# Performance work log

Measured on AMD Instinct MI355X. Metric: run time of the kernel, lower is better.

## Reference

```python
import jax, jax.numpy as jnp
import numpy as np

WS = 8          # window_size
NH = 8          # num_heads
DIM = 512
INNER = 512
CDIM = 128
CINNER = 128
SHIFTED = True
EPS = 1e-6
N = WS * WS     # tokens per window
SCALE = 1.0 / np.sqrt(INNER // NH + CINNER // NH)  # SDPA scale over fused (feat+coord) head dim


def _rmsnorm(x, g):
    return x * jax.lax.rsqrt(jnp.mean(x * x, axis=-1, keepdims=True) + EPS) * g


def _rel_indices():
    idx = np.array([[x, y] for x in range(WS) for y in range(WS)])
    ri = idx[None, :, :] - idx[:, None, :] + WS - 1
    return ri[..., 0], ri[..., 1]


def _shift_mask(Wh, Ww):
    s = WS
    k = s * (s // 2)
    row = np.zeros((N, N), np.float32)
    row[-k:, :-k] = -np.inf
    row[:-k, -k:] = -np.inf
    col = row.reshape(s, s, s, s).transpose(1, 0, 3, 2).reshape(N, N)
    m = np.zeros((Wh, Ww, N, N), np.float32)
    m[:, -1] += row
    m[-1, :] += col
    return jnp.asarray(m)


def setup_inputs() -> dict:
    key = jax.random.key(0)
    ks = jax.random.split(key, 16)
    B, h, w = 4, 128, 128

    def lin(k, fan_in, fan_out):
        return jax.random.normal(k, (fan_in, fan_out), jnp.float32) * (fan_in ** -0.5)

    return {
        "features": jax.random.normal(ks[0], (B, h, w, DIM), jnp.float32),
        "coords": jax.random.normal(ks[1], (B, h, w, CDIM), jnp.float32),
        "w_fqk": lin(ks[2], DIM, 2 * INNER),
        "b_fqk": jnp.zeros((2 * INNER,), jnp.float32),
        "g_fqk": jnp.ones((2 * INNER,), jnp.float32),
        "w_cqk": lin(ks[3], CDIM, 2 * CINNER),
        "b_cqk": jnp.zeros((2 * CINNER,), jnp.float32),
        "g_cqk": jnp.ones((2 * CINNER,), jnp.float32),
        "w_v": lin(ks[4], DIM, INNER),
        "b_v": jnp.zeros((INNER,), jnp.float32),
        "w_out": lin(ks[5], INNER, DIM),
        "b_out": jnp.zeros((DIM,), jnp.float32),
        "pos_emb": jax.random.normal(ks[6], (2 * WS - 1, 2 * WS - 1), jnp.float32),
    }


def reference(features, coords, w_fqk, b_fqk, g_fqk, w_cqk, b_cqk, g_cqk,
              w_v, b_v, w_out, b_out, pos_emb):
    B, h, w, _ = features.shape
    pad_h = (WS - h % WS) % WS
    pad_w = (WS - w % WS) % WS
    H_pad, W_pad = h + pad_h, w + pad_w
    Wh, Ww = H_pad // WS, W_pad // WS

    fqk = _rmsnorm(features @ w_fqk + b_fqk, g_fqk)
    f_q, f_k = jnp.split(fqk, 2, axis=-1)
    cqk = _rmsnorm(coords @ w_cqk + b_cqk, g_cqk)
    c_q, c_k = jnp.split(cqk, 2, axis=-1)
    f_v = features @ w_v + b_v

    def win(t):
        t = jnp.pad(t, ((0, 0), (0, pad_h), (0, pad_w), (0, 0)))
        if SHIFTED:
            t = jnp.roll(t, (-(WS // 2), -(WS // 2)), axis=(1, 2))
        D = t.shape[-1]
        t = t.reshape(B, Wh, WS, Ww, WS, D).transpose(0, 1, 3, 2, 4, 5)
        return t.reshape(B, Wh, Ww, N, D)

    def heads(t):
        D = t.shape[-1]
        return t.reshape(B, Wh, Ww, N, NH, D // NH)

    fq, fk, fv = heads(win(f_q)), heads(win(f_k)), heads(win(f_v))
    cq, ck = heads(win(c_q)), heads(win(c_k))

    # fused feature + coordinate QK scores, per head per window
    scores = (jnp.einsum('bxyqhd,bxykhd->bxyhqk', fq, fk)
              + jnp.einsum('bxyqhd,bxykhd->bxyhqk', cq, ck)) * SCALE

    ri0, ri1 = _rel_indices()
    pos_bias = pos_emb[ri0, ri1]  # (N, N)
    bias = pos_bias[None, None, None, None]
    if SHIFTED:
        bias = bias + _shift_mask(Wh, Ww)[None, :, :, None]
    scores = scores + bias

    attn = jax.nn.softmax(scores, axis=-1)
    out = jnp.einsum('bxyhqk,bxykhd->bxyqhd', attn, fv)
    out = out.reshape(B, Wh, Ww, N, INNER)

    # un-window
    out = out.reshape(B, Wh, Ww, WS, WS, INNER).transpose(0, 1, 3, 2, 4, 5)
    out = out.reshape(B, H_pad, W_pad, INNER)
    if SHIFTED:
        out = jnp.roll(out, (WS // 2, WS // 2), axis=(1, 2))
    out = out[:, :h, :w, :]
    return out @ w_out + b_out
```

## Files before the change

### kernel.cpp

```cpp
#include <hip/hip_runtime.h>
#include <hip/hip_bf16.h>
#include <type_traits>

using bf16 = __hip_bfloat16;
typedef __bf16 bf16x8 __attribute__((ext_vector_type(8)));
typedef float f32x4 __attribute__((ext_vector_type(4)));

static constexpr int TOKENS = 4 * 128 * 128;
#define SCALE_F 0.11180339887498949f
#define EPS_F 1e-6f

__device__ __forceinline__ float u2f(unsigned short u) {
  union { unsigned int i; float f; } c; c.i = (unsigned int)u << 16; return c.f;
}
__device__ __forceinline__ unsigned short f2u(float f) {
  bf16 h = __float2bfloat16(f); return *reinterpret_cast<unsigned short*>(&h);
}
__device__ __forceinline__ float b2f(bf16 v) { return __bfloat162float(v); }
__device__ __forceinline__ int4 cvt8(const float* p) {
  float4 a = ((const float4*)p)[0], b = ((const float4*)p)[1];
  union { int4 i4; unsigned short s[8]; } u;
  u.s[0] = f2u(a.x); u.s[1] = f2u(a.y); u.s[2] = f2u(a.z); u.s[3] = f2u(a.w);
  u.s[4] = f2u(b.x); u.s[5] = f2u(b.y); u.s[6] = f2u(b.z); u.s[7] = f2u(b.w);
  return u.i4;
}
__device__ __forceinline__ void gload16(const bf16* g, bf16* l) {
  __builtin_amdgcn_global_load_lds(
      (const __attribute__((address_space(1))) unsigned int*)g,
      (__attribute__((address_space(3))) unsigned int*)l, 16, 0, 0);
}

__global__ void convert_k(const float* __restrict__ in, bf16* __restrict__ out,
                          long n) {
  long i = ((long)blockIdx.x * 256 + threadIdx.x) * 8;
  long stride = (long)gridDim.x * 256 * 8;
  for (; i < n; i += stride) *(int4*)(out + i) = cvt8(in + i);
}

__global__ void transpose_k(const float* __restrict__ in, bf16* __restrict__ out,
                            int K, int N) {
  int i = blockIdx.x * 256 + threadIdx.x;
  if (i >= K * N) return;
  int k = i / N, n = i - k * N;
  out[(size_t)n * K + k] = __float2bfloat16(in[i]);
}

__global__ void biascat_k(const float* __restrict__ a, const float* __restrict__ b,
                          float* __restrict__ o) {
  int i = blockIdx.x * 256 + threadIdx.x;
  if (i < 1536) o[i] = i < 1024 ? a[i] : b[i - 1024];
}

template <int QF>
__device__ __forceinline__ void mfma16(f32x4 (&acc)[8][4], const bf16x8 (&wfr)[4],
                                       const bf16x8 (&xfr)[4]) {
#pragma unroll
  for (int fi = 0; fi < 4; ++fi)
#pragma unroll
    for (int j = 0; j < 4; ++j)
      acc[QF * 4 + fi][j] =
          __builtin_amdgcn_mfma_f32_16x16x32_bf16(wfr[fi], xfr[j], acc[QF * 4 + fi][j], 0, 0, 0);
}

template <typename TC, int SSNX>
__global__ __launch_bounds__(512, 2) void gemm256_k(
    const bf16* __restrict__ A, const bf16* __restrict__ Wt,
    const float* __restrict__ bias, TC* __restrict__ C,
    float* __restrict__ ssq, int M, int N, int K) {
  extern __shared__ __align__(16) bf16 smem[];
  bf16* sX = smem;
  bf16* sW = smem + 24576;
  const int t = threadIdx.x, lane = t & 63, wave = t >> 6;
  const int wm = wave >> 2, wn = wave & 3;
  const int l15 = lane & 15, kg = lane >> 4;
  const int nwg = gridDim.x * gridDim.y;
  int id = blockIdx.y * gridDim.x + blockIdx.x;
  id = (id & 7) * (nwg >> 3) + (id >> 3);
  const int bx = id % gridDim.x, by = id / gridDim.x;
  const int bm = by * 256, bn = bx * 256;
  f32x4 acc[8][4] = {};

  const int srow = t >> 2;
  const int sw8 = ((t & 3) ^ ((srow >> 1) & 3)) * 8;
  const int sdst = srow * 32 + (t & 3) * 8;
  const int fsw = (kg ^ ((l15 >> 1) & 3)) * 8;

  auto stageX = [&](int buf, int k0) {
    bf16* d = sX + buf * 8192 + sdst;
    gload16(A + (size_t)(bm + srow) * K + k0 + sw8, d);
    gload16(A + (size_t)(bm + 128 + srow) * K + k0 + sw8, d + 4096);
  };
  auto stageW = [&](int buf, int k0) {
    bf16* d = sW + buf * 8192 + sdst;
    gload16(Wt + (size_t)(bn + srow) * K + k0 + sw8, d);
    gload16(Wt + (size_t)(bn + 128 + srow) * K + k0 + sw8, d + 4096);
  };

  const int NT = K >> 5;
  stageX(0, 0); stageW(0, 0); stageX(1, 32); stageW(1, 32);

  int buf = 0;
  for (int u = 0; u < NT; ++u) {
    if (u < NT - 1) asm volatile("s_waitcnt vmcnt(4)" ::: "memory");
    else            asm volatile("s_waitcnt vmcnt(0)" ::: "memory");
    __builtin_amdgcn_s_barrier();
    __builtin_amdgcn_sched_barrier(0);
    int nb = buf + 2; if (nb >= 3) nb -= 3;
    if (u + 2 < NT) stageX(nb, (u + 2) * 32);
    bf16x8 xfr[4], wfr[4];
    const bf16* bX = sX + buf * 8192;
    const bf16* bW = sW + buf * 8192;
#pragma unroll
    for (int j = 0; j < 4; ++j)
      xfr[j] = *(const bf16x8*)(bX + (wn * 64 + j * 16 + l15) * 32 + fsw);
#pragma unroll
    for (int fi = 0; fi < 4; ++fi)
      wfr[fi] = *(const bf16x8*)(bW + (wm * 128 + fi * 16 + l15) * 32 + fsw);
    __builtin_amdgcn_s_setprio(1);
    mfma16<0>(acc, wfr, xfr);
    __builtin_amdgcn_s_setprio(0);
    if (u + 2 < NT) stageW(nb, (u + 2) * 32);
#pragma unroll
    for (int fi = 0; fi < 4; ++fi)
      wfr[fi] = *(const bf16x8*)(bW + (wm * 128 + 64 + fi * 16 + l15) * 32 + fsw);
    __builtin_amdgcn_s_setprio(1);
    mfma16<1>(acc, wfr, xfr);
    __builtin_amdgcn_s_setprio(0);
    buf = (buf == 2) ? 0 : buf + 1;
  }

  float bvi[8][4];
#pragma unroll
  for (int i = 0; i < 8; ++i) {
    float4 b4 = *(const float4*)(bias + bn + wm * 128 + (i >> 2) * 64 + (i & 3) * 16 + kg * 4);
    bvi[i][0] = b4.x; bvi[i][1] = b4.y; bvi[i][2] = b4.z; bvi[i][3] = b4.w;
  }
#pragma unroll
  for (int j = 0; j < 4; ++j) {
    const int token = bm + wn * 64 + j * 16 + l15;
    float ssum = 0.f;
#pragma unroll
    for (int i = 0; i < 8; ++i) {
      float v0 = acc[i][j][0] + bvi[i][0];
      float v1 = acc[i][j][1] + bvi[i][1];
      float v2 = acc[i][j][2] + bvi[i][2];
      float v3 = acc[i][j][3] + bvi[i][3];
      const size_t off = (size_t)token * N + bn + wm * 128 + (i >> 2) * 64 + (i & 3) * 16 + kg * 4;
      if constexpr (std::is_same<TC, float>::value) {
        *(float4*)(C + off) = float4{v0, v1, v2, v3};
      } else {
        ushort4 pk{f2u(v0), f2u(v1), f2u(v2), f2u(v3)};
        *(ushort4*)(C + off) = pk;
      }
      if constexpr (SSNX > 0)
        ssum += v0 * v0 + v1 * v1 + v2 * v2 + v3 * v3;
    }
    if constexpr (SSNX > 0) {
      ssum += __shfl_xor(ssum, 16);
      ssum += __shfl_xor(ssum, 32);
      if (bx < SSNX && kg == 0)
        ssq[(size_t)token * (SSNX * 2) + bx * 2 + wm] = ssum;
    }
  }
}

template <typename TC, int SSNX>
__global__ __launch_bounds__(256) void gemm128_k(
    const bf16* __restrict__ A, const bf16* __restrict__ Wt,
    const float* __restrict__ bias, TC* __restrict__ C,
    float* __restrict__ ssq, int M, int N, int K) {
  __shared__ __align__(16) bf16 sA[2][4096];
  __shared__ __align__(16) bf16 sB[2][4096];
  const int t = threadIdx.x, lane = t & 63, wave = t >> 6;
  const int wr = wave >> 1, wc = wave & 1;
  const int nwg = gridDim.x * gridDim.y;
  int id = blockIdx.y * gridDim.x + blockIdx.x;
  if ((nwg & 7) == 0) id = (id & 7) * (nwg >> 3) + (id >> 3);
  const int bx = id % gridDim.x, by = id / gridDim.x;
  const int bm = by * 128, bn = bx * 128;
  const int l15 = lane & 15, kg = lane >> 4;
  f32x4 acc[4][4] = {};

  const int srow = t >> 2;
  const int ske = ((t & 3) ^ ((srow >> 1) & 3)) * 8;
  const bf16* pA0 = A + (size_t)(bm + srow) * K + ske;
  const bf16* pA1 = A + (size_t)(bm + 64 + srow) * K + ske;
  const bf16* pB0 = Wt + (size_t)(bn + srow) * K + ske;
  const bf16* pB1 = Wt + (size_t)(bn + 64 + srow) * K + ske;
  const int wo = wave * 512;

  gload16(pA0, &sA[0][wo]);
  gload16(pA1, &sA[0][2048 + wo]);
  gload16(pB0, &sB[0][wo]);
  gload16(pB1, &sB[0][2048 + wo]);
  __syncthreads();

  const int nt = K >> 5;
  int cur = 0;
  for (int tt = 0; tt < nt; ++tt) {
    if (tt + 1 < nt) {
      pA0 += 32; pA1 += 32; pB0 += 32; pB1 += 32;
      gload16(pA0, &sA[cur ^ 1][wo]);
      gload16(pA1, &sA[cur ^ 1][2048 + wo]);
      gload16(pB0, &sB[cur ^ 1][wo]);
      gload16(pB1, &sB[cur ^ 1][2048 + wo]);
    }
    bf16x8 wf[4], xf[4];
#pragma unroll
    for (int i = 0; i < 4; ++i) {
      int frow = wc * 64 + i * 16 + l15;
      int xrow = wr * 64 + i * 16 + l15;
      wf[i] = *(const bf16x8*)(&sB[cur][frow * 32 + ((kg ^ ((frow >> 1) & 3)) * 8)]);
      xf[i] = *(const bf16x8*)(&sA[cur][xrow * 32 + ((kg ^ ((xrow >> 1) & 3)) * 8)]);
    }
#pragma unroll
    for (int i = 0; i < 4; ++i)
#pragma unroll
      for (int j = 0; j < 4; ++j)
        acc[i][j] = __builtin_amdgcn_mfma_f32_16x16x32_bf16(wf[i], xf[j], acc[i][j], 0, 0, 0);
    __syncthreads();
    cur ^= 1;
  }

  float bvi[4][4];
#pragma unroll
  for (int i = 0; i < 4; ++i) {
    float4 b4 = *(const float4*)(bias + bn + wc * 64 + i * 16 + kg * 4);
    bvi[i][0] = b4.x; bvi[i][1] = b4.y; bvi[i][2] = b4.z; bvi[i][3] = b4.w;
  }
#pragma unroll
  for (int j = 0; j < 4; ++j) {
    const int token = bm + wr * 64 + j * 16 + l15;
    float ssum = 0.f;
#pragma unroll
    for (int i = 0; i < 4; ++i) {
      float v0 = acc[i][j][0] + bvi[i][0];
      float v1 = acc[i][j][1] + bvi[i][1];
      float v2 = acc[i][j][2] + bvi[i][2];
      float v3 = acc[i][j][3] + bvi[i][3];
      const size_t off = (size_t)token * N + bn + wc * 64 + i * 16 + kg * 4;
      if constexpr (std::is_same<TC, float>::value) {
        *(float4*)(C + off) = float4{v0, v1, v2, v3};
      } else {
        ushort4 pk{f2u(v0), f2u(v1), f2u(v2), f2u(v3)};
        *(ushort4*)(C + off) = pk;
      }
      if constexpr (SSNX > 0)
        ssum += v0 * v0 + v1 * v1 + v2 * v2 + v3 * v3;
    }
    if constexpr (SSNX > 0) {
      ssum += __shfl_xor(ssum, 16);
      ssum += __shfl_xor(ssum, 32);
      if (bx < SSNX && kg == 0)
        ssq[(size_t)token * (SSNX * 2) + bx * 2 + wc] = ssum;
    }
  }
}

__global__ void finalize_rs_k(const float* __restrict__ pf,
                              const float* __restrict__ pc,
                              float* __restrict__ rsf, float* __restrict__ rsc) {
  int i = blockIdx.x * 256 + threadIdx.x;
  if (i >= TOKENS) return;
  float s = 0.f;
#pragma unroll
  for (int j = 0; j < 8; ++j) s += pf[(size_t)i * 8 + j];
  rsf[i] = rsqrtf(s * (1.f / 1024.f) + EPS_F);
  float c = 0.f;
#pragma unroll
  for (int j = 0; j < 4; ++j) c += pc[(size_t)i * 4 + j];
  rsc[i] = rsqrtf(c * (1.f / 256.f) + EPS_F);
}

__global__ __launch_bounds__(256) void attn_mfma_k(
    const bf16* __restrict__ qkv, const bf16* __restrict__ cqk,
    const float* __restrict__ pos, const float* __restrict__ g_fqk,
    const float* __restrict__ g_cqk, const float* __restrict__ rs_f,
    const float* __restrict__ rs_c, bf16* __restrict__ aout) {
  __shared__ __align__(16) bf16 sQ[64][104], sK[64][104];
  __shared__ __align__(16) bf16 sVt[64][72];
  __shared__ __align__(16) bf16 sP[64][72];
  __shared__ float sPos[15][15];
  __shared__ float sRsF[64], sRsC[64];
  const int t = threadIdx.x, lane = t & 63, wave = t >> 6;
  const int head = blockIdx.x & 7;
  const int wid = blockIdx.x >> 3;
  const int wx = wid & 15, wy = (wid >> 4) & 15, b = wid >> 8;

  for (int i = t; i < 225; i += 256) sPos[i / 15][i % 15] = pos[i];
  if (t < 64) {
    const int y = ((wy << 3) + (t >> 3) + 4) & 127;
    const int x = ((wx << 3) + (t & 7) + 4) & 127;
    const size_t tok = ((size_t)b << 14) | (y << 7) | x;
    sRsF[t] = rs_f[tok];
    sRsC[t] = rs_c[tok];
  }
  {
    const int n = t >> 2, p = t & 3;
    const int y = ((wy << 3) + (n >> 3) + 4) & 127;
    const int x = ((wx << 3) + (n & 7) + 4) & 127;
    const size_t tok = ((size_t)b << 14) | (y << 7) | x;
    const bf16* row = qkv + tok * 1536;
    const int4* qp = (const int4*)(row + head * 64 + p * 16);
    ((int4*)&sQ[n][p * 16])[0] = qp[0];
    ((int4*)&sQ[n][p * 16])[1] = qp[1];
    {
      const bf16* kpp = row + 512 + head * 64 + p * 16;
      const float* gq = g_fqk + head * 64 + p * 16;
      const float* gk = g_fqk + 512 + head * 64 + p * 16;
      union { int4 v[2]; unsigned short s[16]; } kt;
#pragma unroll
      for (int i = 0; i < 16; ++i)
        kt.s[i] = f2u(b2f(kpp[i]) * gq[i] * gk[i]);
      ((int4*)&sK[n][p * 16])[0] = kt.v[0];
      ((int4*)&sK[n][p * 16])[1] = kt.v[1];
    }
    const bf16* vp = row + 1024 + head * 64 + p * 16;
#pragma unroll
    for (int i = 0; i < 16; ++i) sVt[p * 16 + i][n] = vp[i];
    const bf16* crow = cqk + tok * 256;
    if (p == 0) {
      const int4* cp = (const int4*)(crow + head * 16);
      ((int4*)&sQ[n][64])[0] = cp[0];
      ((int4*)&sQ[n][64])[1] = cp[1];
    } else if (p == 1) {
      const bf16* ckp = crow + 128 + head * 16;
      const float* gcq = g_cqk + head * 16;
      const float* gck = g_cqk + 128 + head * 16;
      union { int4 v[2]; unsigned short s[16]; } ct;
#pragma unroll
      for (int i = 0; i < 16; ++i)
        ct.s[i] = f2u(b2f(ckp[i]) * gcq[i] * gck[i]);
      ((int4*)&sK[n][64])[0] = ct.v[0];
      ((int4*)&sK[n][64])[1] = ct.v[1];
    } else if (p == 2) {
      ((int4*)&sQ[n][80])[0] = int4{0, 0, 0, 0};
      ((int4*)&sQ[n][80])[1] = int4{0, 0, 0, 0};
    } else {
      ((int4*)&sK[n][80])[0] = int4{0, 0, 0, 0};
      ((int4*)&sK[n][80])[1] = int4{0, 0, 0, 0};
    }
  }
  __syncthreads();

  const int l15 = lane & 15, kg = lane >> 4;
  bf16x8 qa[3];
#pragma unroll
  for (int ko = 0; ko < 3; ++ko)
    qa[ko] = *(const bf16x8*)&sQ[wave * 16 + l15][ko * 32 + kg * 8];
  f32x4 saccf[4] = {}, saccc[4] = {};
#pragma unroll
  for (int j = 0; j < 4; ++j) {
#pragma unroll
    for (int ko = 0; ko < 2; ++ko) {
      bf16x8 kb = *(const bf16x8*)&sK[j * 16 + l15][ko * 32 + kg * 8];
      saccf[j] = __builtin_amdgcn_mfma_f32_16x16x32_bf16(qa[ko], kb, saccf[j], 0, 0, 0);
    }
    bf16x8 kb2 = *(const bf16x8*)&sK[j * 16 + l15][64 + kg * 8];
    saccc[j] = __builtin_amdgcn_mfma_f32_16x16x32_bf16(qa[2], kb2, saccc[j], 0, 0, 0);
  }

  const bool lastx = (wx == 15), lasty = (wy == 15);
  float rqf[4], rqc[4];
#pragma unroll
  for (int r = 0; r < 4; ++r) {
    rqf[r] = sRsF[wave * 16 + kg * 4 + r];
    rqc[r] = sRsC[wave * 16 + kg * 4 + r];
  }
  float sv[4][4], mx[4], sum[4], inv[4];
#pragma unroll
  for (int r = 0; r < 4; ++r) mx[r] = -1e30f;
#pragma unroll
  for (int j = 0; j < 4; ++j) {
    int kcol = j * 16 + l15, kh = kcol >> 3, kw = kcol & 7;
    float rkf = sRsF[kcol], rkc = sRsC[kcol];
#pragma unroll
    for (int r = 0; r < 4; ++r) {
      int q = wave * 16 + kg * 4 + r, qh = q >> 3, qw = q & 7;
      bool msk = (lastx && ((qh >= 4) != (kh >= 4))) ||
                 (lasty && ((qw >= 4) != (kw >= 4)));
      float raw = saccf[j][r] * rqf[r] * rkf + saccc[j][r] * rqc[r] * rkc;
      float val = msk ? -1e30f : raw * SCALE_F + sPos[kh - qh + 7][kw - qw + 7];
      sv[j][r] = val;
      mx[r] = fmaxf(mx[r], val);
    }
  }
#pragma unroll
  for (int m = 1; m < 16; m <<= 1)
#pragma unroll
    for (int r = 0; r < 4; ++r) mx[r] = fmaxf(mx[r], __shfl_xor(mx[r], m));
#pragma unroll
  for (int r = 0; r < 4; ++r) sum[r] = 0.f;
#pragma unroll
  for (int j = 0; j < 4; ++j) {
    int kcol = j * 16 + l15;
#pragma unroll
    for (int r = 0; r < 4; ++r) {
      float e = __expf(sv[j][r] - mx[r]);
      sum[r] += e;
      sP[wave * 16 + kg * 4 + r][kcol] = __float2bfloat16(e);
    }
  }
#pragma unroll
  for (int m = 1; m < 16; m <<= 1)
#pragma unroll
    for (int r = 0; r < 4; ++r) sum[r] += __shfl_xor(sum[r], m);
#pragma unroll
  for (int r = 0; r < 4; ++r) inv[r] = 1.f / sum[r];
  __syncthreads();

  bf16x8 pa[2];
#pragma unroll
  for (int ko = 0; ko < 2; ++ko)
    pa[ko] = *(const bf16x8*)&sP[wave * 16 + l15][ko * 32 + kg * 8];
  f32x4 oacc[4] = {};
#pragma unroll
  for (int jf = 0; jf < 4; ++jf)
#pragma unroll
    for (int ko = 0; ko < 2; ++ko) {
      bf16x8 vb = *(const bf16x8*)&sVt[jf * 16 + l15][ko * 32 + kg * 8];
      oacc[jf] = __builtin_amdgcn_mfma_f32_16x16x32_bf16(pa[ko], vb, oacc[jf], 0, 0, 0);
    }
#pragma unroll
  for (int r = 0; r < 4; ++r) {
    int q = wave * 16 + kg * 4 + r;
    const int y = ((wy << 3) + (q >> 3) + 4) & 127;
    const int x = ((wx << 3) + (q & 7) + 4) & 127;
    const size_t tok = ((size_t)b << 14) | (y << 7) | x;
    bf16* dst = aout + tok * 512 + head * 64;
#pragma unroll
    for (int jf = 0; jf < 4; ++jf)
      dst[jf * 16 + l15] = __float2bfloat16(oacc[jf][r] * inv[r]);
  }
}

extern "C" void kernel_launch(void* const* d_in, const int* in_sizes, int n_in,
                              void* d_out, int out_size, void* d_ws, size_t ws_size,
                              hipStream_t stream) {
  const float* features = (const float*)d_in[0];
  const float* coords   = (const float*)d_in[1];
  const float* w_fqk = (const float*)d_in[2];
  const float* b_fqk = (const float*)d_in[3];
  const float* g_fqk = (const float*)d_in[4];
  const float* w_cqk = (const float*)d_in[5];
  const float* b_cqk = (const float*)d_in[6];
  const float* g_cqk = (const float*)d_in[7];
  const float* w_v   = (const float*)d_in[8];
  const float* b_v   = (const float*)d_in[9];
  const float* w_out = (const float*)d_in[10];
  const float* b_out = (const float*)d_in[11];
  const float* pos_emb = (const float*)d_in[12];
  float* out = (float*)d_out;

  const int M = TOKENS;
  bf16* qkv   = (bf16*)d_ws;
  bf16* cqk   = qkv + (size_t)M * 1536;
  bf16* aout  = cqk + (size_t)M * 256;
  bf16* wcombT = aout + (size_t)M * 512;
  bf16* wcqkT  = wcombT + (size_t)1536 * 512;
  bf16* woutT  = wcqkT + 256 * 128;
  float* bias_comb = (float*)(woutT + 512 * 512);
  float* ssq_f = bias_comb + 1536;
  float* ssq_c = ssq_f + (size_t)M * 8;
  float* rs_f  = ssq_c + (size_t)M * 4;
  float* rs_c  = rs_f + M;
  bf16* fb16 = (bf16*)d_out;
  bf16* cb16 = fb16 + (size_t)M * 512;

  convert_k<<<2048, 256, 0, stream>>>(features, fb16, (long)M * 512);
  convert_k<<<1024, 256, 0, stream>>>(coords, cb16, (long)M * 128);
  transpose_k<<<(512 * 1024 + 255) / 256, 256, 0, stream>>>(w_fqk, wcombT, 512, 1024);
  transpose_k<<<(512 * 512 + 255) / 256, 256, 0, stream>>>(w_v, wcombT + (size_t)1024 * 512, 512, 512);
  transpose_k<<<(128 * 256 + 255) / 256, 256, 0, stream>>>(w_cqk, wcqkT, 128, 256);
  transpose_k<<<(512 * 512 + 255) / 256, 256, 0, stream>>>(w_out, woutT, 512, 512);
  biascat_k<<<6, 256, 0, stream>>>(b_fqk, b_v, bias_comb);

  gemm256_k<bf16, 4><<<dim3(6, 256), 512, 98304, stream>>>(fb16, wcombT, bias_comb, qkv, ssq_f, M, 1536, 512);
  gemm128_k<bf16, 2><<<dim3(2, 512), 256, 0, stream>>>(cb16, wcqkT, b_cqk, cqk, ssq_c, M, 256, 128);
  finalize_rs_k<<<TOKENS / 256, 256, 0, stream>>>(ssq_f, ssq_c, rs_f, rs_c);
  attn_mfma_k<<<4 * 16 * 16 * 8, 256, 0, stream>>>(qkv, cqk, pos_emb, g_fqk, g_cqk, rs_f, rs_c, aout);
  gemm256_k<float, 0><<<dim3(2, 256), 512, 98304, stream>>>(aout, woutT, b_out, out, nullptr, M, 512, 512);
}
```

Baseline: 385.0 us.

## Restructure 256x256 GEMM into double-buffered BK=64 four-phase ping-pong pipeline

Replaces the triple-buffered BK=32 GEMM main loop with a double-buffered BK=64 loop split into four sub-tile phases. Each phase loads one half of the W or X tile from LDS, issues the prefetch for that half of the next tile, and runs its MFMAs, with barriers between phases. The LDS layout changes to 64-element rows with an XOR swizzle, and LDS use grows from 96KB to 128KB per block. The goal is better overlap of global loads with MFMA work and fewer barriers per K element. The cost is more LDS per block, which may limit occupancy below the 2 blocks per CU requested by the launch bounds.

```diff
diff --git a/kernel.cpp b/kernel.cpp
--- a/kernel.cpp
+++ b/kernel.cpp
@@ -51,25 +51,14 @@
   if (i < 1536) o[i] = i < 1024 ? a[i] : b[i - 1024];
 }
 
-template <int QF>
-__device__ __forceinline__ void mfma16(f32x4 (&acc)[8][4], const bf16x8 (&wfr)[4],
-                                       const bf16x8 (&xfr)[4]) {
-#pragma unroll
-  for (int fi = 0; fi < 4; ++fi)
-#pragma unroll
-    for (int j = 0; j < 4; ++j)
-      acc[QF * 4 + fi][j] =
-          __builtin_amdgcn_mfma_f32_16x16x32_bf16(wfr[fi], xfr[j], acc[QF * 4 + fi][j], 0, 0, 0);
-}
-
 template <typename TC, int SSNX>
-__global__ __launch_bounds__(512, 2) void gemm256_k(
+__global__ __launch_bounds__(512, 2) void gemm256p_k(
     const bf16* __restrict__ A, const bf16* __restrict__ Wt,
     const float* __restrict__ bias, TC* __restrict__ C,
     float* __restrict__ ssq, int M, int N, int K) {
   extern __shared__ __align__(16) bf16 smem[];
-  bf16* sX = smem;
-  bf16* sW = smem + 24576;
+  bf16* sW = smem;
+  bf16* sX = smem + 32768;
   const int t = threadIdx.x, lane = t & 63, wave = t >> 6;
   const int wm = wave >> 2, wn = wave & 3;
   const int l15 = lane & 15, kg = lane >> 4;
@@ -80,72 +69,131 @@
   const int bm = by * 256, bn = bx * 256;
   f32x4 acc[8][4] = {};
 
-  const int srow = t >> 2;
-  const int sw8 = ((t & 3) ^ ((srow >> 1) & 3)) * 8;
-  const int sdst = srow * 32 + (t & 3) * 8;
-  const int fsw = (kg ^ ((l15 >> 1) & 3)) * 8;
-
-  auto stageX = [&](int buf, int k0) {
-    bf16* d = sX + buf * 8192 + sdst;
-    gload16(A + (size_t)(bm + srow) * K + k0 + sw8, d);
-    gload16(A + (size_t)(bm + 128 + srow) * K + k0 + sw8, d + 4096);
+  const int lr = t >> 3, ch = t & 7;
+  const int ssw = ((ch ^ (lr & 7)) * 8);
+  const int rsw = (l15 & 7) * 8;
+
+  auto stW = [&](int buf, int fh, int k0) {
+#pragma unroll
+    for (int g = 0; g < 2; ++g)
+      gload16(Wt + (size_t)(bn + g * 128 + fh * 64 + lr) * K + k0 + ssw,
+              sW + buf * 16384 + (fh * 128 + g * 64) * 64 + t * 8);
   };
-  auto stageW = [&](int buf, int k0) {
-    bf16* d = sW + buf * 8192 + sdst;
-    gload16(Wt + (size_t)(bn + srow) * K + k0 + sw8, d);
-    gload16(Wt + (size_t)(bn + 128 + srow) * K + k0 + sw8, d + 4096);
+  auto stX = [&](int buf, int th, int k0) {
+#pragma unroll
+    for (int g = 0; g < 2; ++g)
+      gload16(A + (size_t)(bm + (g * 2 + (lr >> 5)) * 64 + th * 32 + (lr & 31)) * K + k0 + ssw,
+              sX + buf * 16384 + (th * 128 + g * 64) * 64 + t * 8);
   };
-
-  const int NT = K >> 5;
-  stageX(0, 0); stageW(0, 0); stageX(1, 32); stageW(1, 32);
-
-  int buf = 0;
+  auto rdW = [&](int buf, int fh, int i, int ks) {
+    int row = fh * 128 + wm * 64 + i * 16 + l15;
+    return *(const bf16x8*)(sW + buf * 16384 + row * 64 + ((ks * 32 + kg * 8) ^ rsw));
+  };
+  auto rdX = [&](int buf, int th, int j, int ks) {
+    int row = th * 128 + wn * 32 + j * 16 + l15;
+    return *(const bf16x8*)(sX + buf * 16384 + row * 64 + ((ks * 32 + kg * 8) ^ rsw));
+  };
+
+  const int NT = K >> 6;
+  stW(0, 0, 0); stX(0, 0, 0); stX(0, 1, 0); stW(0, 1, 0);
+
+  bf16x8 wfr[4][2], xf0[2][2], xf1[2][2];
   for (int u = 0; u < NT; ++u) {
-    if (u < NT - 1) asm volatile("s_waitcnt vmcnt(4)" ::: "memory");
-    else            asm volatile("s_waitcnt vmcnt(0)" ::: "memory");
+    const int buf = u & 1, nbuf = buf ^ 1, k1 = (u + 1) << 6;
+    const bool pf = (u + 1 < NT);
+    asm volatile("s_waitcnt vmcnt(4)" ::: "memory");
     __builtin_amdgcn_s_barrier();
     __builtin_amdgcn_sched_barrier(0);
-    int nb = buf + 2; if (nb >= 3) nb -= 3;
-    if (u + 2 < NT) stageX(nb, (u + 2) * 32);
-    bf16x8 xfr[4], wfr[4];
-    const bf16* bX = sX + buf * 8192;
-    const bf16* bW = sW + buf * 8192;
-#pragma unroll
-    for (int j = 0; j < 4; ++j)
-      xfr[j] = *(const bf16x8*)(bX + (wn * 64 + j * 16 + l15) * 32 + fsw);
-#pragma unroll
-    for (int fi = 0; fi < 4; ++fi)
-      wfr[fi] = *(const bf16x8*)(bW + (wm * 128 + fi * 16 + l15) * 32 + fsw);
+#pragma unroll
+    for (int i = 0; i < 4; ++i)
+#pragma unroll
+      for (int ks = 0; ks < 2; ++ks) wfr[i][ks] = rdW(buf, 0, i, ks);
+#pragma unroll
+    for (int j = 0; j < 2; ++j)
+#pragma unroll
+      for (int ks = 0; ks < 2; ++ks) xf0[j][ks] = rdX(buf, 0, j, ks);
+    if (pf) { stW(nbuf, 0, k1); stX(nbuf, 0, k1); }
+    asm volatile("s_waitcnt lgkmcnt(0)" ::: "memory");
+    __builtin_amdgcn_sched_barrier(0);
     __builtin_amdgcn_s_setprio(1);
-    mfma16<0>(acc, wfr, xfr);
+#pragma unroll
+    for (int i = 0; i < 4; ++i)
+#pragma unroll
+      for (int j = 0; j < 2; ++j)
+#pragma unroll
+        for (int ks = 0; ks < 2; ++ks)
+          acc[i][j] = __builtin_amdgcn_mfma_f32_16x16x32_bf16(wfr[i][ks], xf0[j][ks], acc[i][j], 0, 0, 0);
     __builtin_amdgcn_s_setprio(0);
-    if (u + 2 < NT) stageW(nb, (u + 2) * 32);
-#pragma unroll
-    for (int fi = 0; fi < 4; ++fi)
-      wfr[fi] = *(const bf16x8*)(bW + (wm * 128 + 64 + fi * 16 + l15) * 32 + fsw);
+    if (pf) asm volatile("s_waitcnt vmcnt(6)" ::: "memory");
+    else    asm volatile("s_waitcnt vmcnt(2)" ::: "memory");
+    __builtin_amdgcn_s_barrier();
+    __builtin_amdgcn_sched_barrier(0);
+#pragma unroll
+    for (int j = 0; j < 2; ++j)
+#pragma unroll
+      for (int ks = 0; ks < 2; ++ks) xf1[j][ks] = rdX(buf, 1, j, ks);
+    if (pf) stX(nbuf, 1, k1);
+    asm volatile("s_waitcnt lgkmcnt(0)" ::: "memory");
+    __builtin_amdgcn_sched_barrier(0);
     __builtin_amdgcn_s_setprio(1);
-    mfma16<1>(acc, wfr, xfr);
+#pragma unroll
+    for (int i = 0; i < 4; ++i)
+#pragma unroll
+      for (int j = 0; j < 2; ++j)
+#pragma unroll
+        for (int ks = 0; ks < 2; ++ks)
+          acc[i][2 + j] = __builtin_amdgcn_mfma_f32_16x16x32_bf16(wfr[i][ks], xf1[j][ks], acc[i][2 + j], 0, 0, 0);
     __builtin_amdgcn_s_setprio(0);
-    buf = (buf == 2) ? 0 : buf + 1;
+    if (pf) asm volatile("s_waitcnt vmcnt(6)" ::: "memory");
+    else    asm volatile("s_waitcnt vmcnt(0)" ::: "memory");
+    __builtin_amdgcn_s_barrier();
+    __builtin_amdgcn_sched_barrier(0);
+#pragma unroll
+    for (int i = 0; i < 4; ++i)
+#pragma unroll
+      for (int ks = 0; ks < 2; ++ks) wfr[i][ks] = rdW(buf, 1, i, ks);
+    if (pf) stW(nbuf, 1, k1);
+    asm volatile("s_waitcnt lgkmcnt(0)" ::: "memory");
+    __builtin_amdgcn_sched_barrier(0);
+    __builtin_amdgcn_s_setprio(1);
+#pragma unroll
+    for (int i = 0; i < 4; ++i)
+#pragma unroll
+      for (int j = 0; j < 2; ++j)
+#pragma unroll
+        for (int ks = 0; ks < 2; ++ks)
+          acc[4 + i][j] = __builtin_amdgcn_mfma_f32_16x16x32_bf16(wfr[i][ks], xf0[j][ks], acc[4 + i][j], 0, 0, 0);
+    __builtin_amdgcn_s_setprio(0);
+    __builtin_amdgcn_s_barrier();
+    __builtin_amdgcn_sched_barrier(0);
+    __builtin_amdgcn_s_setprio(1);
+#pragma unroll
+    for (int i = 0; i < 4; ++i)
+#pragma unroll
+      for (int j = 0; j < 2; ++j)
+#pragma unroll
+        for (int ks = 0; ks < 2; ++ks)
+          acc[4 + i][2 + j] = __builtin_amdgcn_mfma_f32_16x16x32_bf16(wfr[i][ks], xf1[j][ks], acc[4 + i][2 + j], 0, 0, 0);
+    __builtin_amdgcn_s_setprio(0);
   }
 
   float bvi[8][4];
 #pragma unroll
-  for (int i = 0; i < 8; ++i) {
-    float4 b4 = *(const float4*)(bias + bn + wm * 128 + (i >> 2) * 64 + (i & 3) * 16 + kg * 4);
-    bvi[i][0] = b4.x; bvi[i][1] = b4.y; bvi[i][2] = b4.z; bvi[i][3] = b4.w;
-  }
-#pragma unroll
-  for (int j = 0; j < 4; ++j) {
-    const int token = bm + wn * 64 + j * 16 + l15;
+  for (int fi = 0; fi < 8; ++fi) {
+    float4 b4 = *(const float4*)(bias + bn + wm * 128 + (fi >> 2) * 64 + (fi & 3) * 16 + kg * 4);
+    bvi[fi][0] = b4.x; bvi[fi][1] = b4.y; bvi[fi][2] = b4.z; bvi[fi][3] = b4.w;
+  }
+#pragma unroll
+  for (int tj = 0; tj < 4; ++tj) {
+    const int token = bm + wn * 64 + (tj >> 1) * 32 + (tj & 1) * 16 + l15;
     float ssum = 0.f;
 #pragma unroll
-    for (int i = 0; i < 8; ++i) {
-      float v0 = acc[i][j][0] + bvi[i][0];
-      float v1 = acc[i][j][1] + bvi[i][1];
-      float v2 = acc[i][j][2] + bvi[i][2];
-      float v3 = acc[i][j][3] + bvi[i][3];
-      const size_t off = (size_t)token * N + bn + wm * 128 + (i >> 2) * 64 + (i & 3) * 16 + kg * 4;
+    for (int fi = 0; fi < 8; ++fi) {
+      float v0 = acc[fi][tj][0] + bvi[fi][0];
+      float v1 = acc[fi][tj][1] + bvi[fi][1];
+      float v2 = acc[fi][tj][2] + bvi[fi][2];
+      float v3 = acc[fi][tj][3] + bvi[fi][3];
+      const size_t off = (size_t)token * N + bn + wm * 128 + (fi >> 2) * 64 + (fi & 3) * 16 + kg * 4;
       if constexpr (std::is_same<TC, float>::value) {
         *(float4*)(C + off) = float4{v0, v1, v2, v3};
       } else {
@@ -475,9 +523,9 @@
   transpose_k<<<(512 * 512 + 255) / 256, 256, 0, stream>>>(w_out, woutT, 512, 512);
   biascat_k<<<6, 256, 0, stream>>>(b_fqk, b_v, bias_comb);
 
-  gemm256_k<bf16, 4><<<dim3(6, 256), 512, 98304, stream>>>(fb16, wcombT, bias_comb, qkv, ssq_f, M, 1536, 512);
+  gemm256p_k<bf16, 4><<<dim3(6, 256), 512, 131072, stream>>>(fb16, wcombT, bias_comb, qkv, ssq_f, M, 1536, 512);
   gemm128_k<bf16, 2><<<dim3(2, 512), 256, 0, stream>>>(cb16, wcqkT, b_cqk, cqk, ssq_c, M, 256, 128);
   finalize_rs_k<<<TOKENS / 256, 256, 0, stream>>>(ssq_f, ssq_c, rs_f, rs_c);
   attn_mfma_k<<<4 * 16 * 16 * 8, 256, 0, stream>>>(qkv, cqk, pos_emb, g_fqk, g_cqk, rs_f, rs_c, aout);
-  gemm256_k<float, 0><<<dim3(2, 256), 512, 98304, stream>>>(aout, woutT, b_out, out, nullptr, M, 512, 512);
-}
+  gemm256p_k<float, 0><<<dim3(2, 256), 512, 131072, stream>>>(aout, woutT, b_out, out, nullptr, M, 512, 512);
+}
```

New measurement: 374.9 us. -2.6%, faster.
